# Kernel optimization log

Hardware: AMD Instinct MI355X
Metric: run time of the kernel (lower is better)

The kernel has to match this reference:

```python
import jax, jax.numpy as jnp
import numpy as np

NUM_DAYS = 365

# ---- physics model stand-in (SegmentPhysicsModel.compute_current) ----
# source repo not available; use a simple photovoltaic current law:
# I = G * ISC_REF * (1 + ALPHA*(Tcell - T_REF)), channels 0/1 of raw_features.
ISC_REF = 9.0
ALPHA = 0.0005
T_REF = 0.5

def _physics_current(raw):
    G = raw[..., 0:1]
    Tc = raw[..., 1:2]
    return G * ISC_REF * (1.0 + ALPHA * (Tc - T_REF))  # [B,T,1]


def _lstm_layer(x, Wih, Whh, bih, bhh):
    # x: [B,T,D]; PyTorch gate order i,f,g,o
    B = x.shape[0]
    H = Whh.shape[1]
    def step(carry, xt):
        h, c = carry
        g = xt @ Wih.T + h @ Whh.T + bih + bhh
        i, f, gg, o = jnp.split(g, 4, axis=-1)
        c = jax.nn.sigmoid(f) * c + jax.nn.sigmoid(i) * jnp.tanh(gg)
        h = jax.nn.sigmoid(o) * jnp.tanh(c)
        return (h, c), h
    h0 = jnp.zeros((B, H), x.dtype)
    c0 = jnp.zeros((B, H), x.dtype)
    _, ys = jax.lax.scan(step, (h0, c0), jnp.swapaxes(x, 0, 1))
    return jnp.swapaxes(ys, 0, 1)  # [B,T,H]


def _ode_trajectory(h0, W1, b1, W2, b2, W3, b3):
    # dopri5 tableau, fixed step over the t=linspace(0,1,num_days+1) grid
    dt = 1.0 / NUM_DAYS
    def f(h, t):
        inp = jnp.concatenate([h, jnp.reshape(t, (1,))])
        z = jnp.tanh(inp @ W1.T + b1)
        z = jnp.tanh(z @ W2.T + b2)
        return z @ W3.T + b3
    def step(h, t):
        k1 = f(h, t)
        k2 = f(h + dt * (1/5) * k1, t + dt * (1/5))
        k3 = f(h + dt * (3/40 * k1 + 9/40 * k2), t + dt * (3/10))
        k4 = f(h + dt * (44/45 * k1 - 56/15 * k2 + 32/9 * k3), t + dt * (4/5))
        k5 = f(h + dt * (19372/6561 * k1 - 25360/2187 * k2 + 64448/6561 * k3 - 212/729 * k4), t + dt * (8/9))
        k6 = f(h + dt * (9017/3168 * k1 - 355/33 * k2 + 46732/5247 * k3 + 49/176 * k4 - 5103/18656 * k5), t + dt)
        hn = h + dt * (35/384 * k1 + 500/1113 * k3 + 125/192 * k4 - 2187/6784 * k5 + 11/84 * k6)
        return hn, hn
    times = jnp.linspace(0.0, 1.0, NUM_DAYS + 1, dtype=h0.dtype)
    _, traj = jax.lax.scan(step, h0, times[:-1])
    return jnp.concatenate([h0[None, :], traj], axis=0)  # [num_days+1, H]


def setup_inputs() -> dict:
    key = jax.random.key(0)
    ks = jax.random.split(key, 32)
    B, T, F, Fraw = 256, 2048, 32, 4
    HID, HD, FH = 64, 8, 64
    n = lambda k, s, sc=0.05: (jax.random.normal(k, s, dtype=jnp.float32) * sc)
    inp = {
        "X": jax.random.normal(ks[0], (B, T, F), dtype=jnp.float32),
        "day_ids": jax.random.randint(ks[1], (B,), 0, NUM_DAYS + 1),
        "raw_features": jax.random.uniform(ks[2], (B, T, Fraw), dtype=jnp.float32),
        "initial_health": n(ks[3], (HD,), 0.1),
        "ode_W1": n(ks[4], (64, HD + 1)), "ode_b1": jnp.zeros((64,), jnp.float32),
        "ode_W2": n(ks[5], (64, 64)), "ode_b2": jnp.zeros((64,), jnp.float32),
        "ode_W3": n(ks[6], (HD, 64)), "ode_b3": jnp.zeros((HD,), jnp.float32),
        "lstm_Wih0": n(ks[7], (4 * HID, F)), "lstm_Whh0": n(ks[8], (4 * HID, HID)),
        "lstm_bih0": jnp.zeros((4 * HID,), jnp.float32), "lstm_bhh0": jnp.zeros((4 * HID,), jnp.float32),
        "lstm_Wih1": n(ks[9], (4 * HID, HID)), "lstm_Whh1": n(ks[10], (4 * HID, HID)),
        "lstm_bih1": jnp.zeros((4 * HID,), jnp.float32), "lstm_bhh1": jnp.zeros((4 * HID,), jnp.float32),
        "head_decay_weight": n(ks[11], (HD,), 0.01), "head_decay_bias": jnp.zeros((1,), jnp.float32),
        "fus_W1": n(ks[12], (FH, HID + HD + 1)), "fus_b1": jnp.zeros((FH,), jnp.float32),
        "fus_W2": n(ks[13], (FH, FH)), "fus_b2": jnp.zeros((FH,), jnp.float32),
        "res_W1": n(ks[14], (FH // 2, FH)), "res_b1": jnp.zeros((FH // 2,), jnp.float32),
        "res_W2": n(ks[15], (1, FH // 2)), "res_b2": jnp.zeros((1,), jnp.float32),
    }
    return inp


def reference(X, day_ids, raw_features, initial_health, ode_W1, ode_b1, ode_W2, ode_b2, ode_W3, ode_b3, lstm_Wih0, lstm_Whh0, lstm_bih0, lstm_bhh0, lstm_Wih1, lstm_Whh1, lstm_bih1, lstm_bhh1, head_decay_weight, head_decay_bias, fus_W1, fus_b1, fus_W2, fus_b2, res_W1, res_b1, res_W2, res_b2):
    B, T, _ = X.shape
    # LSTM encoder (2 layers)
    env_seq = _lstm_layer(X, lstm_Wih0, lstm_Whh0, lstm_bih0, lstm_bhh0)
    env_seq = _lstm_layer(env_seq, lstm_Wih1, lstm_Whh1, lstm_bih1, lstm_bhh1)
    # health table is detached (traj.detach()) in the original -> stop_gradient
    traj = jax.lax.stop_gradient(_ode_trajectory(initial_health, ode_W1, ode_b1, ode_W2, ode_b2, ode_W3, ode_b3))
    health = traj[day_ids]                                   # [B, H]
    health_seq = jnp.broadcast_to(health[:, None, :], (B, T, health.shape[-1]))
    raw_D = jnp.sum(health_seq * head_decay_weight, axis=-1, keepdims=True) + head_decay_bias
    D = jax.nn.sigmoid(raw_D)                                # [B,T,1]
    I_phys = _physics_current(raw_features)                  # [B,T,1]
    I_base = D * I_phys
    z = jnp.concatenate([env_seq, health_seq, I_phys], axis=-1)  # [B,T,73]
    feat = jax.nn.relu(z @ fus_W1.T + fus_b1)
    feat = jax.nn.relu(feat @ fus_W2.T + fus_b2)
    r = jax.nn.relu(feat @ res_W1.T + res_b1) @ res_W2.T + res_b2
    I_pred = I_base + r
    return (I_pred, I_phys, I_base, D, r, health_seq)
```

## Files before the change

### kernel.cpp

```cpp
#include <hip/hip_runtime.h>
#include <hip/hip_bf16.h>
#include <cstdint>
#include <cstddef>

typedef unsigned int uint;
typedef unsigned short ushort;
typedef _Float16 half2_t __attribute__((ext_vector_type(2)));

#define BATCH 256
#define SEQT  2048
#define FIN   32
#define HID   64
#define FH    64
#define NTOT  (BATCH*SEQT)

enum : int {
  O_B0   = 0,
  O_B1   = O_B0 + 256,
  O_OW1  = O_B1 + 256,
  O_OB1  = O_OW1 + 64*9,
  O_OW2  = O_OB1 + 64,
  O_OB2  = O_OW2 + 64*64,
  O_OW3  = O_OB2 + 64,
  O_OB3  = O_OW3 + 8*64,
  O_OH0  = O_OB3 + 8,
  O_FW1  = O_OH0 + 8,
  O_FB1  = O_FW1 + 64*73,
  O_FW2  = O_FB1 + 64,
  O_FB2  = O_FW2 + 64*64,
  O_RW1  = O_FB2 + 64,
  O_RB1  = O_RW1 + 32*64,
  O_RW2  = O_RB1 + 32,
  O_RB2  = O_RW2 + 32,
  O_HW   = O_RB2 + 1,
  O_HB   = O_HW + 8,
  O_TRAJ = O_HB + 1,
  WS_F32_END = O_TRAJ + 366*8,
  H_WIH0 = WS_F32_END,
  H_WHH0 = H_WIH0 + 256*16,
  H_WIH1 = H_WHH0 + 256*32,
  H_WHH1 = H_WIH1 + 256*32,
  WS_END2 = H_WHH1 + 256*32
};

#define O_FLAG_BYTE  (500*1024)
#define ENV_BYTE_OFF (512*1024)

__device__ __forceinline__ float blo(uint u){ return __uint_as_float(u<<16); }
__device__ __forceinline__ float bhi(uint u){ return __uint_as_float(u & 0xffff0000u); }
__device__ __forceinline__ ushort f2b(float x){
  uint u = __float_as_uint(x);
  uint r = u + 0x7fffu + ((u>>16)&1u);
  return (ushort)(r>>16);
}
__device__ __forceinline__ float sigm(float x){ return 1.0f/(1.0f+__expf(-x)); }
__device__ __forceinline__ float tanh_fast(float x){
  x = fminf(10.0f, fmaxf(-10.0f, x));
  float e = __expf(-2.0f*x);
  return (1.0f - e)/(1.0f + e);
}
__device__ __forceinline__ void wsync(){
  __builtin_amdgcn_wave_barrier();
  __threadfence_block();
  __builtin_amdgcn_wave_barrier();
}
__device__ __forceinline__ uint pkh2(float a, float b){
  half2_t h; h.x=(_Float16)a; h.y=(_Float16)b;
  return __builtin_bit_cast(uint, h);
}
__device__ __forceinline__ half2_t uph(uint u){ return __builtin_bit_cast(half2_t, u); }
__device__ __forceinline__ ushort hbits(float x){ return __builtin_bit_cast(ushort, (_Float16)x); }

#if __has_builtin(__builtin_amdgcn_fdot2)
__device__ __forceinline__ float FDOT2(half2_t a, half2_t b, float c){
  return __builtin_amdgcn_fdot2(a, b, c, false);
}
#else
__device__ __forceinline__ float FDOT2(half2_t a, half2_t b, float c){
  return c + (float)a.x*(float)b.x + (float)a.y*(float)b.y;
}
#endif

__global__ void detect_kernel(const uint* __restrict__ X, int* __restrict__ flagp) {
  if (threadIdx.x == 0) {
    int cnt = 0;
    for (int i=0;i<512;i++){
      uint e = (X[i]>>23)&0xFFu;
      cnt += (e>=97u && e<=157u) ? 1 : 0;
    }
    *flagp = (cnt >= 300) ? 1 : 0;
  }
}

struct Ptrs { const void* p[28]; };

__global__ void prep_kernel(Ptrs ptrs, float* __restrict__ ws, const int* __restrict__ flagp) {
  const int flag = *flagp;
  const int tid = blockIdx.x*blockDim.x + threadIdx.x;
  const int nth = gridDim.x*blockDim.x;
  auto cv = [&](int dst, int srcidx, int n){
    if (flag) {
      const float* s = (const float*)ptrs.p[srcidx];
      for (int i=tid;i<n;i+=nth) ws[dst+i] = s[i];
    } else {
      const ushort* s = (const ushort*)ptrs.p[srcidx];
      for (int i=tid;i<n;i+=nth) ws[dst+i] = __uint_as_float(((uint)s[i])<<16);
    }
  };
  auto rd = [&](int srcidx, int i)->float{
    if (flag) return ((const float*)ptrs.p[srcidx])[i];
    return __uint_as_float(((uint)((const ushort*)ptrs.p[srcidx])[i])<<16);
  };
  auto cvh = [&](int dstw, int srcidx, int n2){
    uint* d = (uint*)ws;
    if (flag) {
      const float* s = (const float*)ptrs.p[srcidx];
      for (int i=tid;i<n2;i+=nth) d[dstw+i] = pkh2(s[2*i], s[2*i+1]);
    } else {
      const uint* s = (const uint*)ptrs.p[srcidx];
      for (int i=tid;i<n2;i+=nth){ uint u=s[i]; d[dstw+i] = pkh2(blo(u), bhi(u)); }
    }
  };
  cvh(H_WIH0,10,4096); cvh(H_WHH0,11,8192); cvh(H_WIH1,14,8192); cvh(H_WHH1,15,8192);
  for (int i=tid;i<256;i+=nth) ws[O_B0+i] = rd(12,i) + rd(13,i);
  for (int i=tid;i<256;i+=nth) ws[O_B1+i] = rd(16,i) + rd(17,i);
  cv(O_OW1,4,576); cv(O_OB1,5,64); cv(O_OW2,6,4096); cv(O_OB2,7,64);
  cv(O_OW3,8,512); cv(O_OB3,9,8);  cv(O_OH0,3,8);
  cv(O_FW1,20,4672); cv(O_FB1,21,64); cv(O_FW2,22,4096); cv(O_FB2,23,64);
  cv(O_RW1,24,2048); cv(O_RB1,25,32); cv(O_RW2,26,32); cv(O_RB2,27,1);
  cv(O_HW,18,8); cv(O_HB,19,1);
}

__device__ void ode_wave(float* __restrict__ ws, float* sbuf) {
  const int lane = threadIdx.x;
  float* sZ1 = sbuf;
  float* sZ2 = sbuf + 64;
  float* sK  = sbuf + 128;

  float w1[9];
#pragma unroll
  for (int k=0;k<9;k++) w1[k]=ws[O_OW1+lane*9+k];
  const float b1 = ws[O_OB1+lane];
  float w2[64];
#pragma unroll
  for (int k=0;k<64;k++) w2[k]=ws[O_OW2+lane*64+k];
  const float b2 = ws[O_OB2+lane];
  const int m = lane>>3, s = lane&7;
  float w3[8];
#pragma unroll
  for (int k=0;k<8;k++) w3[k]=ws[O_OW3+m*64+s*8+k];
  const float b3m = ws[O_OB3+m];

  float h[8];
#pragma unroll
  for (int k=0;k<8;k++) h[k]=ws[O_OH0+k];

  {
    float sel = h[0];
#pragma unroll
    for (int i=1;i<8;i++) sel = (lane==i)? h[i] : sel;
    if (lane<8) ws[O_TRAJ+lane]=sel;
  }

  const float dt = 1.0f/365.0f;
  float k1[8],k2[8],k3[8],k4[8],k5[8],k6[8],ht[8];

  auto feval = [&](const float* hin, float te, float* kout) {
    float a = b1;
#pragma unroll
    for (int k=0;k<8;k++) a += w1[k]*hin[k];
    a += w1[8]*te;
    sZ1[lane] = tanh_fast(a);
    wsync();
    float acc = b2;
    {
      const float4* z4 = (const float4*)sZ1;
#pragma unroll
      for (int k=0;k<16;k++){ float4 v=z4[k];
        acc += w2[4*k]*v.x + w2[4*k+1]*v.y + w2[4*k+2]*v.z + w2[4*k+3]*v.w; }
    }
    sZ2[lane] = tanh_fast(acc);
    wsync();
    float part;
    {
      const float4* q = (const float4*)(sZ2 + s*8);
      float4 p0=q[0], p1=q[1];
      part = w3[0]*p0.x + w3[1]*p0.y + w3[2]*p0.z + w3[3]*p0.w
           + w3[4]*p1.x + w3[5]*p1.y + w3[6]*p1.z + w3[7]*p1.w;
    }
    part += __shfl_xor(part, 1);
    part += __shfl_xor(part, 2);
    part += __shfl_xor(part, 4);
    if (s==0) sK[m] = part + b3m;
    wsync();
    {
      const float4* kk = (const float4*)sK;
      float4 a0=kk[0], a1=kk[1];
      kout[0]=a0.x; kout[1]=a0.y; kout[2]=a0.z; kout[3]=a0.w;
      kout[4]=a1.x; kout[5]=a1.y; kout[6]=a1.z; kout[7]=a1.w;
    }
    wsync();
  };

  for (int d=0; d<365; d++) {
    float t0 = (float)d * dt;
    feval(h, t0, k1);
#pragma unroll
    for (int i=0;i<8;i++) ht[i] = h[i] + dt*(0.2f*k1[i]);
    feval(ht, t0 + 0.2f*dt, k2);
#pragma unroll
    for (int i=0;i<8;i++) ht[i] = h[i] + dt*((3.0f/40.0f)*k1[i] + (9.0f/40.0f)*k2[i]);
    feval(ht, t0 + 0.3f*dt, k3);
#pragma unroll
    for (int i=0;i<8;i++) ht[i] = h[i] + dt*((44.0f/45.0f)*k1[i] - (56.0f/15.0f)*k2[i] + (32.0f/9.0f)*k3[i]);
    feval(ht, t0 + 0.8f*dt, k4);
#pragma unroll
    for (int i=0;i<8;i++) ht[i] = h[i] + dt*((19372.0f/6561.0f)*k1[i] - (25360.0f/2187.0f)*k2[i]
                                   + (64448.0f/6561.0f)*k3[i] - (212.0f/729.0f)*k4[i]);
    feval(ht, t0 + (8.0f/9.0f)*dt, k5);
#pragma unroll
    for (int i=0;i<8;i++) ht[i] = h[i] + dt*((9017.0f/3168.0f)*k1[i] - (355.0f/33.0f)*k2[i]
                                   + (46732.0f/5247.0f)*k3[i] + (49.0f/176.0f)*k4[i]
                                   - (5103.0f/18656.0f)*k5[i]);
    feval(ht, t0 + dt, k6);
#pragma unroll
    for (int i=0;i<8;i++) h[i] += dt*((35.0f/384.0f)*k1[i] + (500.0f/1113.0f)*k3[i]
                                   + (125.0f/192.0f)*k4[i] - (2187.0f/6784.0f)*k5[i]
                                   + (11.0f/84.0f)*k6[i]);
    float sel = h[0];
#pragma unroll
    for (int i=1;i<8;i++) sel = (lane==i)? h[i] : sel;
    if (lane<8) ws[O_TRAJ + (d+1)*8 + lane] = sel;
  }
}

#define XCHUNK 128

__global__ __launch_bounds__(256, 1) void lstm_ode_kernel(const void* __restrict__ Xv,
                                                          float* __restrict__ ws,
                                                          ushort* __restrict__ env,
                                                          const int* __restrict__ flagp,
                                                          int b0, int runOde, int nb) {
  __shared__ __align__(16) uint  sxu[XCHUNK*16];
  __shared__ __align__(16) uint  sh1u[32];
  __shared__ __align__(16) uint  sh2u[32];
  __shared__ __align__(16) float sgA[256];
  __shared__ __align__(16) float sgB[256];

  if ((int)blockIdx.x == nb) {
    if (runOde && threadIdx.x < 64) ode_wave(ws, (float*)sxu);
    return;
  }

  const int flag = *flagp;
  const int b = b0 + blockIdx.x;
  const int j = threadIdx.x;
  const uint* wsu = (const uint*)ws;

  uint wx0[16], wh0[32], wh1[32], ww1[32];
  {
    const uint4* p = (const uint4*)(wsu + H_WIH0 + j*16);
#pragma unroll
    for (int q=0;q<4;q++){ uint4 v=p[q]; wx0[4*q]=v.x; wx0[4*q+1]=v.y; wx0[4*q+2]=v.z; wx0[4*q+3]=v.w; }
  }
  {
    const uint4* p = (const uint4*)(wsu + H_WHH0 + j*32);
#pragma unroll
    for (int q=0;q<8;q++){ uint4 v=p[q]; wh0[4*q]=v.x; wh0[4*q+1]=v.y; wh0[4*q+2]=v.z; wh0[4*q+3]=v.w; }
  }
  {
    const uint4* p = (const uint4*)(wsu + H_WIH1 + j*32);
#pragma unroll
    for (int q=0;q<8;q++){ uint4 v=p[q]; wh1[4*q]=v.x; wh1[4*q+1]=v.y; wh1[4*q+2]=v.z; wh1[4*q+3]=v.w; }
  }
  {
    const uint4* p = (const uint4*)(wsu + H_WHH1 + j*32);
#pragma unroll
    for (int q=0;q<8;q++){ uint4 v=p[q]; ww1[4*q]=v.x; ww1[4*q+1]=v.y; ww1[4*q+2]=v.z; ww1[4*q+3]=v.w; }
  }
  const float bias0 = ws[O_B0+j];
  const float bias1 = ws[O_B1+j];
  float cst = 0.0f;
  if (j < 32) { sh1u[j]=0u; sh2u[j]=0u; }
  const uint*   xrow_b = (const uint*)Xv + (size_t)b*SEQT*(FIN/2);
  const float2* xrow_f = (const float2*)((const float*)Xv + (size_t)b*SEQT*FIN);
  ushort* erow = env + (size_t)blockIdx.x*SEQT*HID;
  __syncthreads();

  for (int t=0; t<=SEQT; ++t) {
    if ((t & (XCHUNK-1)) == 0 && t < SEQT) {
      if (flag) {
        const float2* xc = xrow_f + t*(FIN/2);
#pragma unroll
        for (int it=0; it<(XCHUNK*16)/256; it++){
          int idx = it*256 + j;
          float2 v = xc[idx];
          sxu[idx] = pkh2(v.x, v.y);
        }
      } else {
        const uint* xc = xrow_b + t*(FIN/2);
#pragma unroll
        for (int it=0; it<(XCHUNK*16)/256; it++){
          int idx = it*256 + j;
          uint u = xc[idx];
          sxu[idx] = pkh2(blo(u), bhi(u));
        }
      }
      __syncthreads();
    }
    const int tt = t & (XCHUNK-1);

    uint h1r[32];
    {
      const uint4* p = (const uint4*)sh1u;
#pragma unroll
      for (int q=0;q<8;q++){ uint4 v=p[q]; h1r[4*q]=v.x; h1r[4*q+1]=v.y; h1r[4*q+2]=v.z; h1r[4*q+3]=v.w; }
    }
    uint h2r[32];
    {
      const uint4* p = (const uint4*)sh2u;
#pragma unroll
      for (int q=0;q<8;q++){ uint4 v=p[q]; h2r[4*q]=v.x; h2r[4*q+1]=v.y; h2r[4*q+2]=v.z; h2r[4*q+3]=v.w; }
    }
    if (t < SEQT) {
      uint xr[16];
      const uint4* p = (const uint4*)(sxu + tt*16);
#pragma unroll
      for (int q=0;q<4;q++){ uint4 v=p[q]; xr[4*q]=v.x; xr[4*q+1]=v.y; xr[4*q+2]=v.z; xr[4*q+3]=v.w; }
      float a[4] = {bias0, 0.0f, 0.0f, 0.0f};
#pragma unroll
      for (int k=0;k<16;k++) a[k&3] = FDOT2(uph(wx0[k]), uph(xr[k]), a[k&3]);
#pragma unroll
      for (int k=0;k<32;k++) a[k&3] = FDOT2(uph(wh0[k]), uph(h1r[k]), a[k&3]);
      sgA[j] = (a[0]+a[1])+(a[2]+a[3]);
    }
    if (t >= 1) {
      float c[4] = {bias1, 0.0f, 0.0f, 0.0f};
#pragma unroll
      for (int k=0;k<32;k++) c[k&3] = FDOT2(uph(wh1[k]), uph(h1r[k]), c[k&3]);
#pragma unroll
      for (int k=0;k<32;k++) c[k&3] = FDOT2(uph(ww1[k]), uph(h2r[k]), c[k&3]);
      sgB[j] = (c[0]+c[1])+(c[2]+c[3]);
    }
    __syncthreads();

    if (t < SEQT && j < HID) {
      float gi=sgA[j], gf=sgA[HID+j], gg=sgA[2*HID+j], go=sgA[3*HID+j];
      cst = sigm(gf)*cst + sigm(gi)*tanh_fast(gg);
      float h1 = sigm(go)*tanh_fast(cst);
      ((ushort*)sh1u)[j] = hbits(h1);
    } else if (t >= 1 && j >= HID && j < 2*HID) {
      int u = j - HID;
      float gi=sgB[u], gf=sgB[HID+u], gg=sgB[2*HID+u], go=sgB[3*HID+u];
      cst = sigm(gf)*cst + sigm(gi)*tanh_fast(gg);
      float h2 = sigm(go)*tanh_fast(cst);
      ((ushort*)sh2u)[u] = hbits(h2);
      erow[(size_t)(t-1)*HID + u] = f2b(h2);
    }
    __syncthreads();
  }
}

__global__ __launch_bounds__(256) void fuse_kernel(const ushort* __restrict__ envb,
                                                   const float* __restrict__ ws,
                                                   const int* __restrict__ day_ids,
                                                   const void* __restrict__ rawv,
                                                   void* __restrict__ outv,
                                                   const int* __restrict__ flagp,
                                                   int b0, int nb) {
  const int flag = *flagp;
  const int eloc = blockIdx.x*256 + threadIdx.x;
  const int bloc = eloc >> 11;
  const int b = b0 + bloc;
  const size_t ge = (size_t)b*SEQT + (eloc & 2047);

  int day = day_ids[b];
  day = day < 0 ? 0 : (day > 365 ? 365 : day);
  float hl[8];
#pragma unroll
  for (int i=0;i<8;i++) hl[i] = ws[O_TRAJ + day*8 + i];
  float rawD = ws[O_HB];
#pragma unroll
  for (int i=0;i<8;i++) rawD += hl[i]*ws[O_HW+i];
  const float Dv = sigm(rawD);

  float z[HID];
  {
    const uint4* ev = (const uint4*)(envb + (size_t)eloc*HID);
#pragma unroll
    for (int q=0;q<8;q++){
      uint4 u = ev[q];
      z[8*q+0]=blo(u.x); z[8*q+1]=bhi(u.x);
      z[8*q+2]=blo(u.y); z[8*q+3]=bhi(u.y);
      z[8*q+4]=blo(u.z); z[8*q+5]=bhi(u.z);
      z[8*q+6]=blo(u.w); z[8*q+7]=bhi(u.w);
    }
  }
  float G, Tc;
  if (flag) {
    float2 fr = ((const float2*)rawv)[ge*2];
    G = fr.x; Tc = fr.y;
  } else {
    uint gr = ((const uint*)rawv)[ge*2];
    G = blo(gr); Tc = bhi(gr);
  }
  const float Ip = G*9.0f*(1.0f + 0.0005f*(Tc-0.5f));

  float f1[FH];
#pragma unroll
  for (int jj=0;jj<FH;jj++){
    const float* wr = ws + O_FW1 + jj*73;
    float a = ws[O_FB1+jj];
#pragma unroll
    for (int k=0;k<HID;k++) a += wr[k]*z[k];
#pragma unroll
    for (int i=0;i<8;i++) a += wr[HID+i]*hl[i];
    a += wr[72]*Ip;
    f1[jj] = fmaxf(a,0.0f);
  }
  float f2[FH];
#pragma unroll
  for (int jj=0;jj<FH;jj++){
    const float* wr = ws + O_FW2 + jj*FH;
    float a = ws[O_FB2+jj];
#pragma unroll
    for (int k=0;k<FH;k++) a += wr[k]*f1[k];
    f2[jj] = fmaxf(a,0.0f);
  }
  float racc = ws[O_RB2];
#pragma unroll
  for (int mm=0;mm<32;mm++){
    const float* wr = ws + O_RW1 + mm*FH;
    float a = ws[O_RB1+mm];
#pragma unroll
    for (int k=0;k<FH;k++) a += wr[k]*f2[k];
    racc += ws[O_RW2+mm]*fmaxf(a,0.0f);
  }
  const float Ib = Dv*Ip;
  const float Ipred = Ib + racc;

  if (flag) {
    float* o = (float*)outv;
    o[ge] = Ipred; o[NTOT+ge] = Ip; o[(size_t)2*NTOT+ge] = Ib;
    o[(size_t)3*NTOT+ge] = Dv; o[(size_t)4*NTOT+ge] = racc;
    float4* hp = (float4*)(o + (size_t)5*NTOT + ge*8);
    hp[0] = make_float4(hl[0],hl[1],hl[2],hl[3]);
    hp[1] = make_float4(hl[4],hl[5],hl[6],hl[7]);
  } else {
    ushort* o = (ushort*)outv;
    o[ge] = f2b(Ipred); o[NTOT+ge] = f2b(Ip); o[(size_t)2*NTOT+ge] = f2b(Ib);
    o[(size_t)3*NTOT+ge] = f2b(Dv); o[(size_t)4*NTOT+ge] = f2b(racc);
    uint4 hsv;
    hsv.x = (uint)f2b(hl[0]) | ((uint)f2b(hl[1])<<16);
    hsv.y = (uint)f2b(hl[2]) | ((uint)f2b(hl[3])<<16);
    hsv.z = (uint)f2b(hl[4]) | ((uint)f2b(hl[5])<<16);
    hsv.w = (uint)f2b(hl[6]) | ((uint)f2b(hl[7])<<16);
    *((uint4*)(o + (size_t)5*NTOT + ge*8)) = hsv;
  }
}

extern "C" void kernel_launch(void* const* d_in, const int* in_sizes, int n_in,
                              void* d_out, int out_size, void* d_ws, size_t ws_size,
                              hipStream_t stream) {
  (void)in_sizes; (void)out_size;
  float* wsf = (float*)d_ws;
  int* flagp = (int*)((char*)d_ws + O_FLAG_BYTE);
  ushort* env = (ushort*)((char*)d_ws + ENV_BYTE_OFF);
  Ptrs pa;
  for (int i=0;i<28;i++) pa.p[i] = (i<n_in) ? d_in[i] : d_in[0];

  int S = 1;
  while (S < 128) {
    size_t need = (size_t)ENV_BYTE_OFF + (size_t)(BATCH/S)*SEQT*HID*2;
    if (need <= ws_size) break;
    S <<= 1;
  }
  const int nb = BATCH / S;

  detect_kernel<<<1, 64, 0, stream>>>((const uint*)d_in[0], flagp);
  prep_kernel<<<128, 256, 0, stream>>>(pa, wsf, flagp);
  for (int s=0; s<S; s++) {
    lstm_ode_kernel<<<nb+1, 256, 0, stream>>>(d_in[0], wsf, env, flagp,
                                              s*nb, (s==0)?1:0, nb);
    fuse_kernel<<<nb*(SEQT/256), 256, 0, stream>>>(env, wsf, (const int*)d_in[1],
                                                   d_in[2], d_out, flagp, s*nb, nb);
  }
}
```

Measured before the change: 2.691 ms.

## Broadcast hidden state via readlane and buffer LSTM outputs in LDS

Each lane now loads one dword of the hidden state and the input row from shared memory, and the values are broadcast across the wave with readlane. This replaces the per-thread vector LDS reads of the full h1, h2 and x vectors. The layer-2 outputs are written to an LDS history buffer and flushed to global memory in coalesced 128-step chunks, instead of scattered 2-byte stores every step. The shared loop also computes the layer-0 and layer-1 gates from the same broadcast h1 value. This aims to cut LDS bandwidth and global store overhead on the serial recurrence, at the cost of extra LDS space and flush work.

```diff
diff --git a/kernel.cpp b/kernel.cpp
--- a/kernel.cpp
+++ b/kernel.cpp
@@ -242,10 +242,10 @@
                                                           const int* __restrict__ flagp,
                                                           int b0, int runOde, int nb) {
   __shared__ __align__(16) uint  sxu[XCHUNK*16];
-  __shared__ __align__(16) uint  sh1u[32];
-  __shared__ __align__(16) uint  sh2u[32];
+  __shared__ __align__(16) uint  sHH[64];
   __shared__ __align__(16) float sgA[256];
   __shared__ __align__(16) float sgB[256];
+  __shared__ __align__(16) uint  shist[XCHUNK*32];
 
   if ((int)blockIdx.x == nb) {
     if (runOde && threadIdx.x < 64) ode_wave(ws, (float*)sxu);
@@ -255,6 +255,7 @@
   const int flag = *flagp;
   const int b = b0 + blockIdx.x;
   const int j = threadIdx.x;
+  const int l = j & 63;
   const uint* wsu = (const uint*)ws;
 
   uint wx0[16], wh0[32], wh1[32], ww1[32];
@@ -281,11 +282,19 @@
   const float bias0 = ws[O_B0+j];
   const float bias1 = ws[O_B1+j];
   float cst = 0.0f;
-  if (j < 32) { sh1u[j]=0u; sh2u[j]=0u; }
+  if (j < 64) sHH[j] = 0u;
   const uint*   xrow_b = (const uint*)Xv + (size_t)b*SEQT*(FIN/2);
   const float2* xrow_f = (const float2*)((const float*)Xv + (size_t)b*SEQT*FIN);
-  ushort* erow = env + (size_t)blockIdx.x*SEQT*HID;
+  uint* erow_u = (uint*)env + (size_t)blockIdx.x*SEQT*32;
   __syncthreads();
+
+  auto flush_hist = [&](int baseT){
+#pragma unroll
+    for (int i=0;i<16;i++){
+      int idx = i*256 + j;
+      erow_u[(size_t)(baseT + (idx>>5))*32 + (idx&31)] = shist[idx];
+    }
+  };
 
   for (int t=0; t<=SEQT; ++t) {
     if ((t & (XCHUNK-1)) == 0 && t < SEQT) {
@@ -308,57 +317,58 @@
       }
       __syncthreads();
     }
+    if ((t & (XCHUNK-1)) == 1 && t > 1) {
+      flush_hist(t-129);
+    }
     const int tt = t & (XCHUNK-1);
 
-    uint h1r[32];
-    {
-      const uint4* p = (const uint4*)sh1u;
-#pragma unroll
-      for (int q=0;q<8;q++){ uint4 v=p[q]; h1r[4*q]=v.x; h1r[4*q+1]=v.y; h1r[4*q+2]=v.z; h1r[4*q+3]=v.w; }
-    }
-    uint h2r[32];
-    {
-      const uint4* p = (const uint4*)sh2u;
-#pragma unroll
-      for (int q=0;q<8;q++){ uint4 v=p[q]; h2r[4*q]=v.x; h2r[4*q+1]=v.y; h2r[4*q+2]=v.z; h2r[4*q+3]=v.w; }
-    }
+    uint vh = sHH[l];
+    uint vx = sxu[tt*16 + (l&15)];
+    float a0, a1;
     if (t < SEQT) {
-      uint xr[16];
-      const uint4* p = (const uint4*)(sxu + tt*16);
-#pragma unroll
-      for (int q=0;q<4;q++){ uint4 v=p[q]; xr[4*q]=v.x; xr[4*q+1]=v.y; xr[4*q+2]=v.z; xr[4*q+3]=v.w; }
-      float a[4] = {bias0, 0.0f, 0.0f, 0.0f};
-#pragma unroll
-      for (int k=0;k<16;k++) a[k&3] = FDOT2(uph(wx0[k]), uph(xr[k]), a[k&3]);
-#pragma unroll
-      for (int k=0;k<32;k++) a[k&3] = FDOT2(uph(wh0[k]), uph(h1r[k]), a[k&3]);
-      sgA[j] = (a[0]+a[1])+(a[2]+a[3]);
-    }
-    if (t >= 1) {
-      float c[4] = {bias1, 0.0f, 0.0f, 0.0f};
-#pragma unroll
-      for (int k=0;k<32;k++) c[k&3] = FDOT2(uph(wh1[k]), uph(h1r[k]), c[k&3]);
-#pragma unroll
-      for (int k=0;k<32;k++) c[k&3] = FDOT2(uph(ww1[k]), uph(h2r[k]), c[k&3]);
-      sgB[j] = (c[0]+c[1])+(c[2]+c[3]);
-    }
+      a0 = bias0; a1 = 0.0f;
+#pragma unroll
+      for (int k=0;k<16;k++){
+        uint s = __builtin_amdgcn_readlane(vx, k);
+        float& acc = (k&1) ? a1 : a0;
+        acc = FDOT2(uph(wx0[k]), uph(s), acc);
+      }
+    } else { a0 = 0.0f; a1 = 0.0f; }
+    float c0 = bias1, c1 = 0.0f;
+#pragma unroll
+    for (int k=0;k<32;k++){
+      uint s = __builtin_amdgcn_readlane(vh, k);
+      float& accA = (k&1) ? a1 : a0;
+      float& accC = (k&1) ? c1 : c0;
+      accA = FDOT2(uph(wh0[k]), uph(s), accA);
+      accC = FDOT2(uph(wh1[k]), uph(s), accC);
+    }
+#pragma unroll
+    for (int k=0;k<32;k++){
+      uint s = __builtin_amdgcn_readlane(vh, 32+k);
+      float& accC = (k&1) ? c1 : c0;
+      accC = FDOT2(uph(ww1[k]), uph(s), accC);
+    }
+    if (t < SEQT) sgA[j] = a0 + a1;
+    if (t >= 1)   sgB[j] = c0 + c1;
     __syncthreads();
 
     if (t < SEQT && j < HID) {
       float gi=sgA[j], gf=sgA[HID+j], gg=sgA[2*HID+j], go=sgA[3*HID+j];
       cst = sigm(gf)*cst + sigm(gi)*tanh_fast(gg);
       float h1 = sigm(go)*tanh_fast(cst);
-      ((ushort*)sh1u)[j] = hbits(h1);
+      ((ushort*)sHH)[j] = hbits(h1);
     } else if (t >= 1 && j >= HID && j < 2*HID) {
       int u = j - HID;
       float gi=sgB[u], gf=sgB[HID+u], gg=sgB[2*HID+u], go=sgB[3*HID+u];
       cst = sigm(gf)*cst + sigm(gi)*tanh_fast(gg);
       float h2 = sigm(go)*tanh_fast(cst);
-      ((ushort*)sh2u)[u] = hbits(h2);
-      erow[(size_t)(t-1)*HID + u] = f2b(h2);
+      ((ushort*)sHH)[64 + u] = hbits(h2);
+      ((ushort*)shist)[((t-1)&(XCHUNK-1))*64 + u] = f2b(h2);
     }
     __syncthreads();
   }
+  flush_hist(SEQT-XCHUNK);
 }
 
 __global__ __launch_bounds__(256) void fuse_kernel(const ushort* __restrict__ envb,
```

Result: slower. 2.756 ms (+2.4%).

## Pipeline LSTM layers across three waves with LDS ring buffers and flags

Applied to the files above, without the earlier changes.

Replaces the lock-step 256-thread LSTM kernel, which needed two block barriers per timestep, with a 192-thread producer/consumer pipeline. Wave 0 runs layer-0, wave 1 computes the layer-1 input projection, and wave 2 runs the layer-1 recurrence. They communicate through LDS ring buffers guarded by spin-wait counters, and h is broadcast with readlane. The env output is now stored as fp16 instead of bf16, and fuse_kernel decodes it to match. This removes per-step block syncs and lets the two layers overlap in time, at the cost of more registers per wave and reliance on volatile LDS flag ordering for correctness.

```diff
diff --git a/kernel.cpp b/kernel.cpp
--- a/kernel.cpp
+++ b/kernel.cpp
@@ -69,15 +69,20 @@
   return __builtin_bit_cast(uint, h);
 }
 __device__ __forceinline__ half2_t uph(uint u){ return __builtin_bit_cast(half2_t, u); }
-__device__ __forceinline__ ushort hbits(float x){ return __builtin_bit_cast(ushort, (_Float16)x); }
+__device__ __forceinline__ int hbits(float x){
+  return (int)__builtin_bit_cast(ushort, (_Float16)x) & 0xFFFF;
+}
+#define WAIT_LGKM0() __builtin_amdgcn_s_waitcnt(0xC07F)
+#define MEMBAR()     asm volatile("" ::: "memory")
 
 #if __has_builtin(__builtin_amdgcn_fdot2)
-__device__ __forceinline__ float FDOT2(half2_t a, half2_t b, float c){
-  return __builtin_amdgcn_fdot2(a, b, c, false);
+__device__ __forceinline__ float FDOT2(uint a, uint b, float c){
+  return __builtin_amdgcn_fdot2(uph(a), uph(b), c, false);
 }
 #else
-__device__ __forceinline__ float FDOT2(half2_t a, half2_t b, float c){
-  return c + (float)a.x*(float)b.x + (float)a.y*(float)b.y;
+__device__ __forceinline__ float FDOT2(uint a, uint b, float c){
+  half2_t x = uph(a), y = uph(b);
+  return c + (float)x.x*(float)y.x + (float)x.y*(float)y.y;
 }
 #endif
 
@@ -234,130 +239,167 @@
   }
 }
 
-#define XCHUNK 128
-
-__global__ __launch_bounds__(256, 1) void lstm_ode_kernel(const void* __restrict__ Xv,
-                                                          float* __restrict__ ws,
-                                                          ushort* __restrict__ env,
-                                                          const int* __restrict__ flagp,
-                                                          int b0, int runOde, int nb) {
-  __shared__ __align__(16) uint  sxu[XCHUNK*16];
-  __shared__ __align__(16) uint  sh1u[32];
-  __shared__ __align__(16) uint  sh2u[32];
-  __shared__ __align__(16) float sgA[256];
-  __shared__ __align__(16) float sgB[256];
+#define RH 64
+#define RP 16
+
+__global__ __launch_bounds__(192) void lstm_pipe_kernel(const void* __restrict__ Xv,
+                                                        float* __restrict__ ws,
+                                                        ushort* __restrict__ env,
+                                                        const int* __restrict__ flagp,
+                                                        int b0, int runOde, int nb) {
+  __shared__ __align__(16) uint  sx[128*16];
+  __shared__ __align__(16) uint  ringH[RH*32];
+  __shared__ __align__(16) float ringP[RP*256];
+  __shared__ int cnts[4];
 
   if ((int)blockIdx.x == nb) {
-    if (runOde && threadIdx.x < 64) ode_wave(ws, (float*)sxu);
+    if (runOde && threadIdx.x < 64) ode_wave(ws, (float*)sx);
     return;
   }
 
   const int flag = *flagp;
   const int b = b0 + blockIdx.x;
-  const int j = threadIdx.x;
+  const int wave = threadIdx.x >> 6;
+  const int lane = threadIdx.x & 63;
   const uint* wsu = (const uint*)ws;
-
-  uint wx0[16], wh0[32], wh1[32], ww1[32];
-  {
-    const uint4* p = (const uint4*)(wsu + H_WIH0 + j*16);
-#pragma unroll
-    for (int q=0;q<4;q++){ uint4 v=p[q]; wx0[4*q]=v.x; wx0[4*q+1]=v.y; wx0[4*q+2]=v.z; wx0[4*q+3]=v.w; }
-  }
-  {
-    const uint4* p = (const uint4*)(wsu + H_WHH0 + j*32);
-#pragma unroll
-    for (int q=0;q<8;q++){ uint4 v=p[q]; wh0[4*q]=v.x; wh0[4*q+1]=v.y; wh0[4*q+2]=v.z; wh0[4*q+3]=v.w; }
-  }
-  {
-    const uint4* p = (const uint4*)(wsu + H_WIH1 + j*32);
-#pragma unroll
-    for (int q=0;q<8;q++){ uint4 v=p[q]; wh1[4*q]=v.x; wh1[4*q+1]=v.y; wh1[4*q+2]=v.z; wh1[4*q+3]=v.w; }
-  }
-  {
-    const uint4* p = (const uint4*)(wsu + H_WHH1 + j*32);
-#pragma unroll
-    for (int q=0;q<8;q++){ uint4 v=p[q]; ww1[4*q]=v.x; ww1[4*q+1]=v.y; ww1[4*q+2]=v.z; ww1[4*q+3]=v.w; }
-  }
-  const float bias0 = ws[O_B0+j];
-  const float bias1 = ws[O_B1+j];
-  float cst = 0.0f;
-  if (j < 32) { sh1u[j]=0u; sh2u[j]=0u; }
-  const uint*   xrow_b = (const uint*)Xv + (size_t)b*SEQT*(FIN/2);
-  const float2* xrow_f = (const float2*)((const float*)Xv + (size_t)b*SEQT*FIN);
-  ushort* erow = env + (size_t)blockIdx.x*SEQT*HID;
+  if (threadIdx.x < 4) cnts[threadIdx.x] = -1;
   __syncthreads();
-
-  for (int t=0; t<=SEQT; ++t) {
-    if ((t & (XCHUNK-1)) == 0 && t < SEQT) {
-      if (flag) {
-        const float2* xc = xrow_f + t*(FIN/2);
-#pragma unroll
-        for (int it=0; it<(XCHUNK*16)/256; it++){
-          int idx = it*256 + j;
-          float2 v = xc[idx];
-          sxu[idx] = pkh2(v.x, v.y);
-        }
-      } else {
-        const uint* xc = xrow_b + t*(FIN/2);
-#pragma unroll
-        for (int it=0; it<(XCHUNK*16)/256; it++){
-          int idx = it*256 + j;
-          uint u = xc[idx];
-          sxu[idx] = pkh2(blo(u), bhi(u));
+  volatile int* vc = cnts;
+
+  if (wave == 0) {
+    uint wx[4][16], wh[4][32];
+    float bias[4];
+#pragma unroll
+    for (int g=0; g<4; g++){
+      const uint4* p = (const uint4*)(wsu + H_WIH0 + (g*64+lane)*16);
+#pragma unroll
+      for (int q=0;q<4;q++){ uint4 v=p[q]; wx[g][4*q]=v.x; wx[g][4*q+1]=v.y; wx[g][4*q+2]=v.z; wx[g][4*q+3]=v.w; }
+      const uint4* r = (const uint4*)(wsu + H_WHH0 + (g*64+lane)*32);
+#pragma unroll
+      for (int q=0;q<8;q++){ uint4 v=r[q]; wh[g][4*q]=v.x; wh[g][4*q+1]=v.y; wh[g][4*q+2]=v.z; wh[g][4*q+3]=v.w; }
+      bias[g] = ws[O_B0 + g*64 + lane];
+    }
+    const uint4*   xb4 = (const uint4*)((const uint*)Xv + (size_t)b*SEQT*16);
+    const float4*  xf4 = (const float4*)((const float*)Xv + (size_t)b*SEQT*FIN);
+    float c1 = 0.0f;
+    uint vh1pk = 0u;
+
+    for (int t=0; t<SEQT; ++t) {
+      if ((t & 127) == 0) {
+        if (flag) {
+#pragma unroll
+          for (int i=0;i<16;i++){
+            float4 v = xf4[(size_t)(t>>2)*8  + i*64 + lane];
+            uint2 w; w.x = pkh2(v.x,v.y); w.y = pkh2(v.z,v.w);
+            ((uint2*)sx)[i*64 + lane] = w;
+          }
+        } else {
+#pragma unroll
+          for (int i=0;i<8;i++){
+            uint4 u = xb4[(size_t)t*4 + i*64 + lane];
+            uint4 w;
+            w.x = pkh2(blo(u.x), bhi(u.x)); w.y = pkh2(blo(u.y), bhi(u.y));
+            w.z = pkh2(blo(u.z), bhi(u.z)); w.w = pkh2(blo(u.w), bhi(u.w));
+            ((uint4*)sx)[i*64 + lane] = w;
+          }
         }
       }
-      __syncthreads();
-    }
-    const int tt = t & (XCHUNK-1);
-
-    uint h1r[32];
-    {
-      const uint4* p = (const uint4*)sh1u;
-#pragma unroll
-      for (int q=0;q<8;q++){ uint4 v=p[q]; h1r[4*q]=v.x; h1r[4*q+1]=v.y; h1r[4*q+2]=v.z; h1r[4*q+3]=v.w; }
-    }
-    uint h2r[32];
-    {
-      const uint4* p = (const uint4*)sh2u;
-#pragma unroll
-      for (int q=0;q<8;q++){ uint4 v=p[q]; h2r[4*q]=v.x; h2r[4*q+1]=v.y; h2r[4*q+2]=v.z; h2r[4*q+3]=v.w; }
-    }
-    if (t < SEQT) {
-      uint xr[16];
-      const uint4* p = (const uint4*)(sxu + tt*16);
-#pragma unroll
-      for (int q=0;q<4;q++){ uint4 v=p[q]; xr[4*q]=v.x; xr[4*q+1]=v.y; xr[4*q+2]=v.z; xr[4*q+3]=v.w; }
-      float a[4] = {bias0, 0.0f, 0.0f, 0.0f};
-#pragma unroll
-      for (int k=0;k<16;k++) a[k&3] = FDOT2(uph(wx0[k]), uph(xr[k]), a[k&3]);
-#pragma unroll
-      for (int k=0;k<32;k++) a[k&3] = FDOT2(uph(wh0[k]), uph(h1r[k]), a[k&3]);
-      sgA[j] = (a[0]+a[1])+(a[2]+a[3]);
-    }
-    if (t >= 1) {
-      float c[4] = {bias1, 0.0f, 0.0f, 0.0f};
-#pragma unroll
-      for (int k=0;k<32;k++) c[k&3] = FDOT2(uph(wh1[k]), uph(h1r[k]), c[k&3]);
-#pragma unroll
-      for (int k=0;k<32;k++) c[k&3] = FDOT2(uph(ww1[k]), uph(h2r[k]), c[k&3]);
-      sgB[j] = (c[0]+c[1])+(c[2]+c[3]);
-    }
-    __syncthreads();
-
-    if (t < SEQT && j < HID) {
-      float gi=sgA[j], gf=sgA[HID+j], gg=sgA[2*HID+j], go=sgA[3*HID+j];
-      cst = sigm(gf)*cst + sigm(gi)*tanh_fast(gg);
-      float h1 = sigm(go)*tanh_fast(cst);
-      ((ushort*)sh1u)[j] = hbits(h1);
-    } else if (t >= 1 && j >= HID && j < 2*HID) {
-      int u = j - HID;
-      float gi=sgB[u], gf=sgB[HID+u], gg=sgB[2*HID+u], go=sgB[3*HID+u];
-      cst = sigm(gf)*cst + sigm(gi)*tanh_fast(gg);
-      float h2 = sigm(go)*tanh_fast(cst);
-      ((ushort*)sh2u)[u] = hbits(h2);
-      erow[(size_t)(t-1)*HID + u] = f2b(h2);
-    }
-    __syncthreads();
+      while (vc[1] < t - RH) { __builtin_amdgcn_s_sleep(1); }
+
+      uint vx = sx[(t&127)*16 + (lane&15)];
+      float a[4] = {bias[0], bias[1], bias[2], bias[3]};
+      float z[4] = {0.f,0.f,0.f,0.f};
+#pragma unroll
+      for (int k=0;k<16;k++){
+        uint s = (uint)__builtin_amdgcn_readlane((int)vx, k);
+        if (k&1){ z[0]=FDOT2(wx[0][k],s,z[0]); z[1]=FDOT2(wx[1][k],s,z[1]);
+                  z[2]=FDOT2(wx[2][k],s,z[2]); z[3]=FDOT2(wx[3][k],s,z[3]); }
+        else    { a[0]=FDOT2(wx[0][k],s,a[0]); a[1]=FDOT2(wx[1][k],s,a[1]);
+                  a[2]=FDOT2(wx[2][k],s,a[2]); a[3]=FDOT2(wx[3][k],s,a[3]); }
+      }
+#pragma unroll
+      for (int k=0;k<32;k++){
+        uint s = (uint)__builtin_amdgcn_readlane((int)vh1pk, k);
+        if (k&1){ z[0]=FDOT2(wh[0][k],s,z[0]); z[1]=FDOT2(wh[1][k],s,z[1]);
+                  z[2]=FDOT2(wh[2][k],s,z[2]); z[3]=FDOT2(wh[3][k],s,z[3]); }
+        else    { a[0]=FDOT2(wh[0][k],s,a[0]); a[1]=FDOT2(wh[1][k],s,a[1]);
+                  a[2]=FDOT2(wh[2][k],s,a[2]); a[3]=FDOT2(wh[3][k],s,a[3]); }
+      }
+      float gi=a[0]+z[0], gf=a[1]+z[1], gg=a[2]+z[2], go=a[3]+z[3];
+      c1 = sigm(gf)*c1 + sigm(gi)*tanh_fast(gg);
+      float h1 = sigm(go)*tanh_fast(c1);
+      int hb = hbits(h1);
+      uint lo = (uint)__shfl(hb, 2*lane);
+      uint hi = (uint)__shfl(hb, 2*lane+1);
+      vh1pk = lo | (hi<<16);
+      if (lane < 32) ringH[(t&(RH-1))*32 + lane] = vh1pk;
+      WAIT_LGKM0(); MEMBAR();
+      if (lane == 0) vc[0] = t;
+    }
+  } else if (wave == 1) {
+    uint wi[4][32];
+    float bias1[4];
+#pragma unroll
+    for (int g=0; g<4; g++){
+      const uint4* p = (const uint4*)(wsu + H_WIH1 + (g*64+lane)*32);
+#pragma unroll
+      for (int q=0;q<8;q++){ uint4 v=p[q]; wi[g][4*q]=v.x; wi[g][4*q+1]=v.y; wi[g][4*q+2]=v.z; wi[g][4*q+3]=v.w; }
+      bias1[g] = ws[O_B1 + g*64 + lane];
+    }
+    for (int t=0; t<SEQT; ++t) {
+      while (vc[0] < t)      { __builtin_amdgcn_s_sleep(1); }
+      while (vc[2] < t - RP) { __builtin_amdgcn_s_sleep(1); }
+      MEMBAR();
+      uint vh = ringH[(t&(RH-1))*32 + (lane&31)];
+      float p0=bias1[0], p1=bias1[1], p2=bias1[2], p3=bias1[3];
+      float q0=0.f, q1=0.f, q2=0.f, q3=0.f;
+#pragma unroll
+      for (int k=0;k<32;k++){
+        uint s = (uint)__builtin_amdgcn_readlane((int)vh, k);
+        if (k&1){ q0=FDOT2(wi[0][k],s,q0); q1=FDOT2(wi[1][k],s,q1);
+                  q2=FDOT2(wi[2][k],s,q2); q3=FDOT2(wi[3][k],s,q3); }
+        else    { p0=FDOT2(wi[0][k],s,p0); p1=FDOT2(wi[1][k],s,p1);
+                  p2=FDOT2(wi[2][k],s,p2); p3=FDOT2(wi[3][k],s,p3); }
+      }
+      ((float4*)(ringP + (t&(RP-1))*256))[lane] = make_float4(p0+q0, p1+q1, p2+q2, p3+q3);
+      WAIT_LGKM0(); MEMBAR();
+      if (lane == 0) vc[1] = t;
+    }
+  } else {
+    uint wh2[4][32];
+#pragma unroll
+    for (int g=0; g<4; g++){
+      const uint4* p = (const uint4*)(wsu + H_WHH1 + (g*64+lane)*32);
+#pragma unroll
+      for (int q=0;q<8;q++){ uint4 v=p[q]; wh2[g][4*q]=v.x; wh2[g][4*q+1]=v.y; wh2[g][4*q+2]=v.z; wh2[g][4*q+3]=v.w; }
+    }
+    uint* erow = (uint*)env + (size_t)blockIdx.x*SEQT*32;
+    float c2 = 0.0f;
+    uint vh2pk = 0u;
+    for (int t=0; t<SEQT; ++t) {
+      while (vc[1] < t) { __builtin_amdgcn_s_sleep(1); }
+      MEMBAR();
+      float4 pp = ((const float4*)(ringP + (t&(RP-1))*256))[lane];
+      float a0=0.f,a1=0.f,a2=0.f,a3=0.f, z0=0.f,z1=0.f,z2=0.f,z3=0.f;
+#pragma unroll
+      for (int k=0;k<32;k++){
+        uint s = (uint)__builtin_amdgcn_readlane((int)vh2pk, k);
+        if (k&1){ z0=FDOT2(wh2[0][k],s,z0); z1=FDOT2(wh2[1][k],s,z1);
+                  z2=FDOT2(wh2[2][k],s,z2); z3=FDOT2(wh2[3][k],s,z3); }
+        else    { a0=FDOT2(wh2[0][k],s,a0); a1=FDOT2(wh2[1][k],s,a1);
+                  a2=FDOT2(wh2[2][k],s,a2); a3=FDOT2(wh2[3][k],s,a3); }
+      }
+      float gi=pp.x+a0+z0, gf=pp.y+a1+z1, gg=pp.z+a2+z2, go=pp.w+a3+z3;
+      c2 = sigm(gf)*c2 + sigm(gi)*tanh_fast(gg);
+      float h2 = sigm(go)*tanh_fast(c2);
+      int hb = hbits(h2);
+      uint lo = (uint)__shfl(hb, 2*lane);
+      uint hi = (uint)__shfl(hb, 2*lane+1);
+      vh2pk = lo | (hi<<16);
+      if (lane < 32) erow[(size_t)t*32 + lane] = vh2pk;
+      WAIT_LGKM0(); MEMBAR();
+      if (lane == 0) vc[2] = t;
+    }
   }
 }
 
@@ -390,10 +432,11 @@
 #pragma unroll
     for (int q=0;q<8;q++){
       uint4 u = ev[q];
-      z[8*q+0]=blo(u.x); z[8*q+1]=bhi(u.x);
-      z[8*q+2]=blo(u.y); z[8*q+3]=bhi(u.y);
-      z[8*q+4]=blo(u.z); z[8*q+5]=bhi(u.z);
-      z[8*q+6]=blo(u.w); z[8*q+7]=bhi(u.w);
+      half2_t h0=uph(u.x), h1=uph(u.y), h2=uph(u.z), h3=uph(u.w);
+      z[8*q+0]=(float)h0.x; z[8*q+1]=(float)h0.y;
+      z[8*q+2]=(float)h1.x; z[8*q+3]=(float)h1.y;
+      z[8*q+4]=(float)h2.x; z[8*q+5]=(float)h2.y;
+      z[8*q+6]=(float)h3.x; z[8*q+7]=(float)h3.y;
     }
   }
   float G, Tc;
@@ -480,8 +523,8 @@
   detect_kernel<<<1, 64, 0, stream>>>((const uint*)d_in[0], flagp);
   prep_kernel<<<128, 256, 0, stream>>>(pa, wsf, flagp);
   for (int s=0; s<S; s++) {
-    lstm_ode_kernel<<<nb+1, 256, 0, stream>>>(d_in[0], wsf, env, flagp,
-                                              s*nb, (s==0)?1:0, nb);
+    lstm_pipe_kernel<<<nb+1, 192, 0, stream>>>(d_in[0], wsf, env, flagp,
+                                               s*nb, (s==0)?1:0, nb);
     fuse_kernel<<<nb*(SEQT/256), 256, 0, stream>>>(env, wsf, (const int*)d_in[1],
                                                    d_in[2], d_out, flagp, s*nb, nb);
   }
```

Measured after the change: 2.425 ms. -9.9%, faster.
